# Optimization experiments

Measured on AMD Instinct MI355X. Metric: run time of the kernel, lower is better.

Reference implementation:

```python
import jax, jax.numpy as jnp
import numpy as np

# Each of the 16 soft logic gates op_i(a,b) is linear in the basis {1, a, b, a*b}.
# Row i gives (c_const, c_a, c_b, c_ab) for gate i (standard difflogic ordering,
# gate 3 = A pass-through, gate 1 = AND, gate 6 = XOR, etc.).
_M = jnp.array([
    [0, 0, 0, 0],   # 0: False
    [0, 0, 0, 1],   # 1: a AND b
    [0, 1, 0, -1],  # 2: a AND NOT b
    [0, 1, 0, 0],   # 3: a
    [0, 0, 1, -1],  # 4: NOT a AND b
    [0, 0, 1, 0],   # 5: b
    [0, 1, 1, -2],  # 6: a XOR b
    [0, 1, 1, -1],  # 7: a OR b
    [1, -1, -1, 1], # 8: NOT (a OR b)
    [1, -1, -1, 2], # 9: NOT (a XOR b)
    [1, 0, -1, 0],  # 10: NOT b
    [1, 0, -1, 1],  # 11: a OR NOT b
    [1, -1, 0, 0],  # 12: NOT a
    [1, -1, 0, 1],  # 13: NOT a OR b
    [1, 0, 0, -1],  # 14: NOT (a AND b)
    [1, 0, 0, 0],   # 15: True
], dtype=jnp.float32)

B, C, H, W = 16, 3, 64, 64
K, DEPTH, RF, STRIDE = 32, 4, 5, 1
S = 2 ** DEPTH            # 16 leaf pairs per tree
OUT_H = (H - RF) // STRIDE + 1  # 60
OUT_W = (W - RF) // STRIDE + 1  # 60
P = OUT_H * OUT_W         # 3600 sliding positions


def setup_inputs() -> dict:
    key = jax.random.key(0)
    ks = jax.random.split(key, 12)
    x = jax.random.uniform(ks[0], (B, C, H, W), dtype=jnp.float32)

    # Random (h, w, c) pairs inside the receptive field, per kernel / leaf slot
    # (connections='random'): relative offsets in [0, RF) x [0, RF) x [0, C).
    def rel(k1, k2, k3):
        rh = jax.random.randint(k1, (K, S), 0, RF)
        rw = jax.random.randint(k2, (K, S), 0, RF)
        rc = jax.random.randint(k3, (K, S), 0, C)
        return rh, rw, rc

    rha, rwa, rca = rel(ks[1], ks[2], ks[3])
    rhb, rwb, rcb = rel(ks[4], ks[5], ks[6])

    # Expand relative offsets over all sliding-window positions -> absolute indices.
    oh, ow = jnp.meshgrid(jnp.arange(OUT_H), jnp.arange(OUT_W), indexing='ij')
    oh = (oh.reshape(-1) * STRIDE)[None, :, None]  # (1, P, 1)
    ow = (ow.reshape(-1) * STRIDE)[None, :, None]

    def absolute(rh, rw, rc):
        ah = oh + rh[:, None, :]                       # (K, P, S)
        aw = ow + rw[:, None, :]
        ac = jnp.broadcast_to(rc[:, None, :], (K, P, S))
        return ah.astype(jnp.int32), aw.astype(jnp.int32), ac.astype(jnp.int32)

    ah, aw, ac = absolute(rha, rwa, rca)
    bh, bw, bc = absolute(rhb, rwb, rcb)

    # Gate-selection logits per tree level: level l has 2**(DEPTH-l) gates,
    # each with (K, 16) logits (weight_init='random').
    ws = {}
    for l in range(DEPTH + 1):
        n = 2 ** (DEPTH - l)
        ws[f'w{l}'] = jax.random.normal(ks[7 + l], (n, K, 16), dtype=jnp.float32)

    return dict(x=x, ah=ah, aw=aw, ac=ac, bh=bh, bw=bw, bc=bc, **ws)


def _bin_op(a, b, w):
    """Weighted mix of 16 soft logic gates.

    a, b: (B, K, P, S);  w: (S, K, 16) raw logits, soft_raw = softmax.
    """
    coef = jax.nn.softmax(w, axis=-1) @ _M           # (S, K, 4)
    coef = jnp.transpose(coef, (2, 1, 0))[:, :, None, :]  # (4, K, 1, S)
    return coef[0] + coef[1] * a + coef[2] * b + coef[3] * (a * b)


def reference(x, ah, aw, ac, bh, bw, bc, w0, w1, w2, w3, w4):
    # Level 0: irregular gather of feature pairs over (c, h, w).
    a = x[:, ac, ah, aw]   # (B, K, P, S)
    b = x[:, bc, bh, bw]
    cur = _bin_op(a, b, w0)
    # Higher levels: combine adjacent sibling nodes (even/odd) along node dim.
    for w in (w1, w2, w3, w4):
        cur = _bin_op(cur[..., 0::2], cur[..., 1::2], w)
    # cur: (B, K, P, 1) -> (B, K, OUT_H, OUT_W)
    return cur.reshape(cur.shape[0], cur.shape[1], OUT_H, OUT_W)
```

## Files before the change

### kernel.cpp

```cpp
#include <hip/hip_runtime.h>

#define B_   16
#define C_   3
#define H_   64
#define W_   64
#define K_   32
#define S_   16
#define OH_  60
#define OW_  60
#define P_   3600
#define IMG  (C_*H_*W_)

#define KG   8
#define NKG  (K_/KG)
#define ROWS (C_*5)
#define BPAD 20
#define ROWSTRIDE (W_*BPAD)
#define XLDS (ROWS*ROWSTRIDE)

__device__ __forceinline__ float gate(float4 c, float a, float b) {
    return fmaf(c.w, a * b, fmaf(c.z, b, fmaf(c.y, a, c.x)));
}

__global__ __launch_bounds__(512, 2) void logic_fused_kernel(
    const float* __restrict__ x,
    const int* __restrict__ ah, const int* __restrict__ aw, const int* __restrict__ ac,
    const int* __restrict__ bh, const int* __restrict__ bw, const int* __restrict__ bc,
    const float* __restrict__ w0, const float* __restrict__ w1,
    const float* __restrict__ w2, const float* __restrict__ w3,
    const float* __restrict__ w4,
    float* __restrict__ out)
{
    __shared__ float  xs[XLDS];
    __shared__ float4 cf[KG * 31];
    __shared__ int    bAi[KG * S_], bBi[KG * S_];

    const int oh  = blockIdx.x;
    const int kg  = blockIdx.y;
    const int tid = threadIdx.x;
    const int l   = tid & 63;
    const int wv  = tid >> 6;

    for (int job = wv; job < ROWS * B_; job += 8) {
        int b   = job & 15;
        int row = job >> 4;
        int c   = row / 5, dh = row - c * 5;
        float v = x[((b * C_ + c) * H_ + (oh + dh)) * W_ + l];
        xs[row * ROWSTRIDE + l * BPAD + b] = v;
    }

    if (tid < 256) {
        int node = tid & 31, kk = tid >> 5;
        if (node < 31) {
            int k = kg * KG + kk;
            const float* w; int i;
            if      (node < 16) { w = w0; i = node;      }
            else if (node < 24) { w = w1; i = node - 16; }
            else if (node < 28) { w = w2; i = node - 24; }
            else if (node < 30) { w = w3; i = node - 28; }
            else                { w = w4; i = 0;         }
            const float* src = w + ((size_t)i * K_ + k) * 16;
            float lg[16];
            float m = -1e30f;
#pragma unroll
            for (int s = 0; s < 16; ++s) { lg[s] = src[s]; m = fmaxf(m, lg[s]); }
            float sum = 0.f;
#pragma unroll
            for (int s = 0; s < 16; ++s) { lg[s] = expf(lg[s] - m); sum += lg[s]; }
            float inv = 1.f / sum;
            const float M[16][4] = {
                {0,0,0,0},{0,0,0,1},{0,1,0,-1},{0,1,0,0},
                {0,0,1,-1},{0,0,1,0},{0,1,1,-2},{0,1,1,-1},
                {1,-1,-1,1},{1,-1,-1,2},{1,0,-1,0},{1,0,-1,1},
                {1,-1,0,0},{1,-1,0,1},{1,0,0,-1},{1,0,0,0}};
            float c0 = 0.f, c1 = 0.f, c2 = 0.f, c3 = 0.f;
#pragma unroll
            for (int s = 0; s < 16; ++s) {
                float pr = lg[s] * inv;
                c0 += pr * M[s][0]; c1 += pr * M[s][1];
                c2 += pr * M[s][2]; c3 += pr * M[s][3];
            }
            cf[kk * 31 + node] = make_float4(c0, c1, c2, c3);
        }
    } else {
        int i = tid - 256;
        int s = i & 15, kk = (i >> 4) & 7;
        int k = kg * KG + kk;
        int idx = k * (P_ * 16) + s;
        if (i < 128)
            bAi[kk * 16 + s] = (ac[idx] * 5 + ah[idx]) * ROWSTRIDE + aw[idx] * BPAD;
        else
            bBi[kk * 16 + s] = (bc[idx] * 5 + bh[idx]) * ROWSTRIDE + bw[idx] * BPAD;
    }
    __syncthreads();

    const int k = kg * KG + wv;
    const int e = l >> 4;

    float4 creg[S_];
#pragma unroll
    for (int s = 0; s < S_; ++s) creg[s] = cf[wv * 31 + s];

    int baseA[S_], baseB[S_];
#pragma unroll
    for (int s = 0; s < S_; ++s) {
        baseA[s] = __builtin_amdgcn_readfirstlane(bAi[wv * 16 + s]);
        baseB[s] = __builtin_amdgcn_readfirstlane(bBi[wv * 16 + s]);
    }

    const int obase = k * P_ + oh * OW_;

    for (int q = 0; q < 4; ++q) {
        int ow     = q * 16 + (l & 15);
        int ow_eff = ow < OW_ ? ow : OW_ - 1;
        int lo     = ow_eff * BPAD + e * 4;

        float t[4][8];
#pragma unroll
        for (int i = 0; i < 8; ++i) {
            float4 a0 = *(const float4*)&xs[baseA[2*i]   + lo];
            float4 b0 = *(const float4*)&xs[baseB[2*i]   + lo];
            float4 a1 = *(const float4*)&xs[baseA[2*i+1] + lo];
            float4 b1 = *(const float4*)&xs[baseB[2*i+1] + lo];
            float4 c0 = creg[2*i], c1 = creg[2*i+1];
            float4 d  = cf[wv * 31 + 16 + i];
            {
                float la = gate(c0, a0.x, b0.x), lb = gate(c1, a1.x, b1.x);
                t[0][i] = gate(d, la, lb);
            }
            {
                float la = gate(c0, a0.y, b0.y), lb = gate(c1, a1.y, b1.y);
                t[1][i] = gate(d, la, lb);
            }
            {
                float la = gate(c0, a0.z, b0.z), lb = gate(c1, a1.z, b1.z);
                t[2][i] = gate(d, la, lb);
            }
            {
                float la = gate(c0, a0.w, b0.w), lb = gate(c1, a1.w, b1.w);
                t[3][i] = gate(d, la, lb);
            }
        }
#pragma unroll
        for (int i = 0; i < 4; ++i) {
            float4 c = cf[wv * 31 + 24 + i];
#pragma unroll
            for (int j = 0; j < 4; ++j)
                t[j][i] = gate(c, t[j][2*i], t[j][2*i+1]);
        }
#pragma unroll
        for (int i = 0; i < 2; ++i) {
            float4 c = cf[wv * 31 + 28 + i];
#pragma unroll
            for (int j = 0; j < 4; ++j)
                t[j][i] = gate(c, t[j][2*i], t[j][2*i+1]);
        }
        {
            float4 c = cf[wv * 31 + 30];
            if (ow < OW_) {
#pragma unroll
                for (int j = 0; j < 4; ++j) {
                    float r = gate(c, t[j][0], t[j][1]);
                    out[(size_t)(e * 4 + j) * (K_ * P_) + obase + ow] = r;
                }
            }
        }
    }
}

extern "C" void kernel_launch(void* const* d_in, const int* in_sizes, int n_in,
                              void* d_out, int out_size, void* d_ws, size_t ws_size,
                              hipStream_t stream) {
    const float* x  = (const float*)d_in[0];
    const int* ah = (const int*)d_in[1];
    const int* aw = (const int*)d_in[2];
    const int* ac = (const int*)d_in[3];
    const int* bh = (const int*)d_in[4];
    const int* bw = (const int*)d_in[5];
    const int* bc = (const int*)d_in[6];
    const float* w0 = (const float*)d_in[7];
    const float* w1 = (const float*)d_in[8];
    const float* w2 = (const float*)d_in[9];
    const float* w3 = (const float*)d_in[10];
    const float* w4 = (const float*)d_in[11];
    float* out = (float*)d_out;

    dim3 grid(OH_, NKG);
    logic_fused_kernel<<<grid, 512, 0, stream>>>(x, ah, aw, ac, bh, bw, bc,
                                                 w0, w1, w2, w3, w4, out);
}
```

Baseline: 26.15 us.

## Split batch across blocks and shrink blocks to raise grid parallelism

The grid gains a batch-half dimension and each block now handles 4 kernels instead of 8, using 256 threads instead of 512. Each block stages only 8 batch images into LDS with a tighter padding of 8, so shared memory per block shrinks and more blocks can be resident. Coefficients are now read from LDS on every use instead of being cached in registers, trading register pressure for extra LDS reads. The grid grows from 240 to 960 blocks, which should fill the CUs better, but the x tiles are now loaded redundantly across more blocks.

```diff
diff --git a/kernel.cpp b/kernel.cpp
--- a/kernel.cpp
+++ b/kernel.cpp
@@ -9,23 +9,22 @@
 #define OH_  60
 #define OW_  60
 #define P_   3600
-#define IMG  (C_*H_*W_)
-
-#define KG   8
+
+#define KG   4
 #define NKG  (K_/KG)
 #define ROWS (C_*5)
-#define BPAD 20
-#define ROWSTRIDE (W_*BPAD)
+#define BP   8
+#define ROWSTRIDE (W_*BP)
 #define XLDS (ROWS*ROWSTRIDE)
 
 __device__ __forceinline__ float gate(float4 c, float a, float b) {
     return fmaf(c.w, a * b, fmaf(c.z, b, fmaf(c.y, a, c.x)));
 }
 
-__global__ __launch_bounds__(512, 2) void logic_fused_kernel(
+__global__ __launch_bounds__(256, 4) void logic_fused_kernel(
     const float* __restrict__ x,
     const int* __restrict__ ah, const int* __restrict__ aw, const int* __restrict__ ac,
-    const int* __restrict__ bh, const int* __restrict__ bw, const int* __restrict__ bc,
+    const int* __restrict__ bh_, const int* __restrict__ bw_, const int* __restrict__ bc_,
     const float* __restrict__ w0, const float* __restrict__ w1,
     const float* __restrict__ w2, const float* __restrict__ w3,
     const float* __restrict__ w4,
@@ -36,20 +35,27 @@
     __shared__ int    bAi[KG * S_], bBi[KG * S_];
 
     const int oh  = blockIdx.x;
-    const int kg  = blockIdx.y;
+    const int bh  = blockIdx.y;
+    const int kg  = blockIdx.z;
     const int tid = threadIdx.x;
     const int l   = tid & 63;
     const int wv  = tid >> 6;
 
-    for (int job = wv; job < ROWS * B_; job += 8) {
-        int b   = job & 15;
-        int row = job >> 4;
-        int c   = row / 5, dh = row - c * 5;
-        float v = x[((b * C_ + c) * H_ + (oh + dh)) * W_ + l];
-        xs[row * ROWSTRIDE + l * BPAD + b] = v;
-    }
-
-    if (tid < 256) {
+    {
+        const int b  = l & 7;
+        const int w0 = l >> 3;
+        const int gb = bh * 8 + b;
+        for (int job = wv; job < ROWS * 8; job += 4) {
+            int wb  = job & 7;
+            int row = job >> 3;
+            int c   = row / 5, dh = row - c * 5;
+            int w   = w0 + 8 * wb;
+            xs[row * ROWSTRIDE + w * BP + b] =
+                x[((gb * C_ + c) * H_ + (oh + dh)) * W_ + w];
+        }
+    }
+
+    if (tid < 128) {
         int node = tid & 31, kk = tid >> 5;
         if (node < 31) {
             int k = kg * KG + kk;
@@ -83,23 +89,25 @@
             cf[kk * 31 + node] = make_float4(c0, c1, c2, c3);
         }
     } else {
-        int i = tid - 256;
-        int s = i & 15, kk = (i >> 4) & 7;
-        int k = kg * KG + kk;
-        int idx = k * (P_ * 16) + s;
-        if (i < 128)
-            bAi[kk * 16 + s] = (ac[idx] * 5 + ah[idx]) * ROWSTRIDE + aw[idx] * BPAD;
-        else
-            bBi[kk * 16 + s] = (bc[idx] * 5 + bh[idx]) * ROWSTRIDE + bw[idx] * BPAD;
+        int i = tid - 128;
+        int s = i & 15;
+        if (i < 64) {
+            int kk = i >> 4;
+            int k  = kg * KG + kk;
+            int idx = k * (P_ * 16) + s;
+            bAi[kk * 16 + s] = (ac[idx] * 5 + ah[idx]) * ROWSTRIDE + aw[idx] * BP;
+        } else {
+            int kk = (i - 64) >> 4;
+            int k  = kg * KG + kk;
+            int idx = k * (P_ * 16) + s;
+            bBi[kk * 16 + s] = (bc_[idx] * 5 + bh_[idx]) * ROWSTRIDE + bw_[idx] * BP;
+        }
     }
     __syncthreads();
 
-    const int k = kg * KG + wv;
-    const int e = l >> 4;
-
-    float4 creg[S_];
-#pragma unroll
-    for (int s = 0; s < S_; ++s) creg[s] = cf[wv * 31 + s];
+    const int k   = kg * KG + wv;
+    const int e   = l >> 5;
+    const int owl = l & 31;
 
     int baseA[S_], baseB[S_];
 #pragma unroll
@@ -108,12 +116,13 @@
         baseB[s] = __builtin_amdgcn_readfirstlane(bBi[wv * 16 + s]);
     }
 
+    const float4* cfw = &cf[wv * 31];
     const int obase = k * P_ + oh * OW_;
 
-    for (int q = 0; q < 4; ++q) {
-        int ow     = q * 16 + (l & 15);
+    for (int q = 0; q < 2; ++q) {
+        int ow     = q * 32 + owl;
         int ow_eff = ow < OW_ ? ow : OW_ - 1;
-        int lo     = ow_eff * BPAD + e * 4;
+        int lo     = ow_eff * BP + e * 4;
 
         float t[4][8];
 #pragma unroll
@@ -122,8 +131,8 @@
             float4 b0 = *(const float4*)&xs[baseB[2*i]   + lo];
             float4 a1 = *(const float4*)&xs[baseA[2*i+1] + lo];
             float4 b1 = *(const float4*)&xs[baseB[2*i+1] + lo];
-            float4 c0 = creg[2*i], c1 = creg[2*i+1];
-            float4 d  = cf[wv * 31 + 16 + i];
+            float4 c0 = cfw[2*i], c1 = cfw[2*i+1];
+            float4 d  = cfw[16 + i];
             {
                 float la = gate(c0, a0.x, b0.x), lb = gate(c1, a1.x, b1.x);
                 t[0][i] = gate(d, la, lb);
@@ -143,25 +152,25 @@
         }
 #pragma unroll
         for (int i = 0; i < 4; ++i) {
-            float4 c = cf[wv * 31 + 24 + i];
+            float4 c = cfw[24 + i];
 #pragma unroll
             for (int j = 0; j < 4; ++j)
                 t[j][i] = gate(c, t[j][2*i], t[j][2*i+1]);
         }
 #pragma unroll
         for (int i = 0; i < 2; ++i) {
-            float4 c = cf[wv * 31 + 28 + i];
+            float4 c = cfw[28 + i];
 #pragma unroll
             for (int j = 0; j < 4; ++j)
                 t[j][i] = gate(c, t[j][2*i], t[j][2*i+1]);
         }
         {
-            float4 c = cf[wv * 31 + 30];
+            float4 c = cfw[30];
             if (ow < OW_) {
 #pragma unroll
                 for (int j = 0; j < 4; ++j) {
                     float r = gate(c, t[j][0], t[j][1]);
-                    out[(size_t)(e * 4 + j) * (K_ * P_) + obase + ow] = r;
+                    out[(size_t)(bh * 8 + e * 4 + j) * (K_ * P_) + obase + ow] = r;
                 }
             }
         }
@@ -185,7 +194,7 @@
     const float* w4 = (const float*)d_in[11];
     float* out = (float*)d_out;
 
-    dim3 grid(OH_, NKG);
-    logic_fused_kernel<<<grid, 512, 0, stream>>>(x, ah, aw, ac, bh, bw, bc,
+    dim3 grid(OH_, 2, NKG);
+    logic_fused_kernel<<<grid, 256, 0, stream>>>(x, ah, aw, ac, bh, bw, bc,
                                                  w0, w1, w2, w3, w4, out);
 }
```

Result: slower. 43.38 us (+65.8%).
